# Kernel optimization log

Hardware: AMD Instinct MI355X
Metric: run time of the kernel (lower is better)

The kernel has to match this reference:

```python
import jax, jax.numpy as jnp
import numpy as np

B, S, D, H = 8, 1024, 768, 12
DH = D // H  # per-head dim = 64


def setup_inputs() -> dict:
    key = jax.random.key(0)
    ks = jax.random.split(key, 9)
    scale = 1.0 / np.sqrt(D)
    x = jax.random.normal(ks[0], (B, S, D), dtype=jnp.float32)
    # Per-head projection weights stacked over the head axis [H, D, DH]
    Wq = jax.random.normal(ks[1], (H, D, DH), dtype=jnp.float32) * scale
    bq = jax.random.normal(ks[2], (H, DH), dtype=jnp.float32) * 0.02
    Wk = jax.random.normal(ks[3], (H, D, DH), dtype=jnp.float32) * scale
    bk = jax.random.normal(ks[4], (H, DH), dtype=jnp.float32) * 0.02
    Wv = jax.random.normal(ks[5], (H, D, DH), dtype=jnp.float32) * scale
    bv = jax.random.normal(ks[6], (H, DH), dtype=jnp.float32) * 0.02
    Wo = jax.random.normal(ks[7], (D, D), dtype=jnp.float32) * scale
    bo = jax.random.normal(ks[8], (D,), dtype=jnp.float32) * 0.02
    return {"x": x, "Wq": Wq, "bq": bq, "Wk": Wk, "bk": bk,
            "Wv": Wv, "bv": bv, "Wo": Wo, "bo": bo}


def reference(x, Wq, bq, Wk, bk, Wv, bv, Wo, bo):
    # Batched equivalent of the per-head Python loop: each head has its own
    # Q/K/V linear projections (weights stacked on the head axis).
    q = jnp.einsum('bsd,hde->bhse', x, Wq) + bq[None, :, None, :]
    k = jnp.einsum('bsd,hde->bhse', x, Wk) + bk[None, :, None, :]
    v = jnp.einsum('bsd,hde->bhse', x, Wv) + bv[None, :, None, :]
    scores = jnp.einsum('bhse,bhte->bhst', q, k) / jnp.sqrt(jnp.float32(DH))
    attn = jax.nn.softmax(scores, axis=-1)
    out = jnp.einsum('bhst,bhte->bhse', attn, v)  # [B,H,S,DH]
    # concat heads on last dim -> [B,S,H*DH] = [B,S,D]
    out = out.transpose(0, 2, 1, 3).reshape(B, S, D)
    return out @ Wo.T + bo
```

## Files before the change

kernel.cpp:

```cpp
#include <hip/hip_runtime.h>
#include <hip/hip_bf16.h>


typedef unsigned short u16;
typedef unsigned int u32;
typedef __attribute__((ext_vector_type(8))) short bf16x8;
typedef __attribute__((ext_vector_type(8))) unsigned short u16x8;
typedef __attribute__((ext_vector_type(4))) float f32x4;
typedef __attribute__((ext_vector_type(4))) u32 u32x4;

typedef __attribute__((address_space(1))) const u32* gas_u32;
typedef __attribute__((address_space(3))) u32* las_u32;

#define DEVI __device__ __forceinline__

DEVI u16 f2bf(float f) {
  union { float f; u32 u; } v; v.f = f;
  u32 r = v.u + 0x7fffu + ((v.u >> 16) & 1u);
  return (u16)(r >> 16);
}

DEVI void gll16(const void* g, void* l) {
  __builtin_amdgcn_global_load_lds((gas_u32)g, (las_u32)l, 16, 0, 0);
}

DEVI f32x4 mfma16(bf16x8 a, bf16x8 b, f32x4 c) {
  return __builtin_amdgcn_mfma_f32_16x16x32_bf16(a, b, c, 0, 0, 0);
}

DEVI u32 cvtpk(float lo, float hi) {
  u32 r;
  asm("v_cvt_pk_bf16_f32 %0, %1, %2" : "=v"(r) : "v"(lo), "v"(hi));
  return r;
}

__global__ __launch_bounds__(256) void k_conv(const float* __restrict__ in,
                                              u16* __restrict__ out, int n4) {
  int i = blockIdx.x * 256 + threadIdx.x;
  if (i >= n4) return;
  float4 v = ((const float4*)in)[i];
  ushort4 o;
  o.x = f2bf(v.x); o.y = f2bf(v.y); o.z = f2bf(v.z); o.w = f2bf(v.w);
  ((ushort4*)out)[i] = o;
}

__global__ __launch_bounds__(256) void k_transW(const float* __restrict__ Wq,
                                                const float* __restrict__ Wk,
                                                const float* __restrict__ Wv,
                                                u16* __restrict__ Wtb) {
  __shared__ u16 T[64][65];
  const int th = blockIdx.y;
  const float* W = (th < 12) ? Wq : (th < 24) ? Wk : Wv;
  const int h = th % 12;
  W += (size_t)h * 768 * 64;
  const int k0 = blockIdx.x * 64;
  const int tid = threadIdx.x;
  const int row = tid >> 2, c = tid & 3;
  const float* src = W + (size_t)(k0 + row) * 64 + c * 16;
#pragma unroll
  for (int j = 0; j < 4; ++j) {
    float4 v = ((const float4*)src)[j];
    T[row][c * 16 + j * 4 + 0] = f2bf(v.x);
    T[row][c * 16 + j * 4 + 1] = f2bf(v.y);
    T[row][c * 16 + j * 4 + 2] = f2bf(v.z);
    T[row][c * 16 + j * 4 + 3] = f2bf(v.w);
  }
  __syncthreads();
  const int e = tid >> 2;
  u16* dst = Wtb + ((size_t)th * 64 + e) * 768 + k0 + c * 16;
  alignas(16) u16 tmp[16];
#pragma unroll
  for (int j = 0; j < 16; ++j) tmp[j] = T[c * 16 + j][e];
  *(u16x8*)(dst)     = *(const u16x8*)(tmp);
  *(u16x8*)(dst + 8) = *(const u16x8*)(tmp + 8);
}

template <int MODE>
__global__ __launch_bounds__(256) void k_gemm(const u16* __restrict__ Ab,
                                              const u16* __restrict__ Bb,
                                              const float* __restrict__ bias,
                                              void* __restrict__ outp) {
  __shared__ u16 smem[12288];
  u16* As = smem;
  u16* Bs = smem + 128 * 64;
  const int tid = threadIdx.x;
  const int w = tid >> 6, lane = tid & 63, lq = lane & 15, g = lane >> 4;
  const int wm = w >> 1, wn = w & 1;
  const int m0 = blockIdx.x * 128;
  const int pn = blockIdx.y;
  const u16* Brows = Bb + (size_t)pn * 64 * 768;

  f32x4 acc[4][2];
#pragma unroll
  for (int mf = 0; mf < 4; ++mf)
#pragma unroll
    for (int nf = 0; nf < 2; ++nf) acc[mf][nf] = (f32x4){0.f, 0.f, 0.f, 0.f};

  for (int kt = 0; kt < 12; ++kt) {
    const int kb = kt * 64;
#pragma unroll
    for (int i = 0; i < 4; ++i) {
      int c = w * 4 + i;
      int id = c * 64 + lane;
      int row = id >> 3, cb = id & 7;
      gll16(Ab + (size_t)(m0 + row) * 768 + kb + ((cb ^ (row & 7)) << 3), As + c * 512);
    }
#pragma unroll
    for (int i = 0; i < 2; ++i) {
      int c = w * 2 + i;
      int id = c * 64 + lane;
      int row = id >> 3, cb = id & 7;
      gll16(Brows + (size_t)row * 768 + kb + ((cb ^ (row & 7)) << 3), Bs + c * 512);
    }
    __syncthreads();
#pragma unroll
    for (int kk = 0; kk < 2; ++kk) {
      bf16x8 a[4], b[2];
#pragma unroll
      for (int mf = 0; mf < 4; ++mf) {
        int row = wm * 64 + mf * 16 + lq;
        a[mf] = *(const bf16x8*)(As + row * 64 + (((kk * 64 + g * 16) ^ ((row & 7) << 4)) >> 1));
      }
#pragma unroll
      for (int nf = 0; nf < 2; ++nf) {
        int row = wn * 32 + nf * 16 + lq;
        b[nf] = *(const bf16x8*)(Bs + row * 64 + (((kk * 64 + g * 16) ^ ((row & 7) << 4)) >> 1));
      }
#pragma unroll
      for (int mf = 0; mf < 4; ++mf)
#pragma unroll
        for (int nf = 0; nf < 2; ++nf)
          acc[mf][nf] = mfma16(a[mf], b[nf], acc[mf][nf]);
    }
    __syncthreads();
  }

  if (MODE <= 1) {
    u16* out = (u16*)outp;
    const float qs = (MODE == 0) ? 0.18033688f : 1.0f;
    const int b = m0 >> 10;
#pragma unroll
    for (int nf = 0; nf < 2; ++nf) {
      const int e = wn * 32 + nf * 16 + lq;
      const float bi = bias[pn * 64 + e];
#pragma unroll
      for (int mf = 0; mf < 4; ++mf)
#pragma unroll
        for (int r = 0; r < 4; ++r) {
          int s = (m0 & 1023) + wm * 64 + mf * 16 + 4 * g + r;
          out[((size_t)(b * 12 + pn) * 1024 + s) * 64 + e] = f2bf((acc[mf][nf][r] + bi) * qs);
        }
    }
  } else if (MODE == 2) {
    u16* Ct = smem;
#pragma unroll
    for (int nf = 0; nf < 2; ++nf) {
      const int e = wn * 32 + nf * 16 + lq;
      const float bi = bias[pn * 64 + e];
#pragma unroll
      for (int mf = 0; mf < 4; ++mf)
#pragma unroll
        for (int r = 0; r < 4; ++r) {
          int sl = wm * 64 + mf * 16 + 4 * g + r;
          Ct[e * 136 + sl] = f2bf(acc[mf][nf][r] + bi);
        }
    }
    __syncthreads();
    const int b = m0 >> 10;
    const int er = tid >> 2, cc = tid & 3;
    u16* dst = (u16*)outp + ((size_t)(b * 12 + pn) * 64 + er) * 1024 + (m0 & 1023) + cc * 32;
#pragma unroll
    for (int i = 0; i < 4; ++i)
      *(u16x8*)(dst + i * 8) = *(const u16x8*)(Ct + er * 136 + cc * 32 + i * 8);
  } else {
    float* out = (float*)outp;
#pragma unroll
    for (int nf = 0; nf < 2; ++nf) {
      const int n = pn * 64 + wn * 32 + nf * 16 + lq;
      const float bi = bias[n];
#pragma unroll
      for (int mf = 0; mf < 4; ++mf)
#pragma unroll
        for (int r = 0; r < 4; ++r) {
          int m = m0 + wm * 64 + mf * 16 + 4 * g + r;
          out[(size_t)m * 768 + n] = acc[mf][nf][r] + bi;
        }
    }
  }
}

__global__ __launch_bounds__(256) void k_attn(const u16* __restrict__ Qb,
                                              const u16* __restrict__ Kb,
                                              const u16* __restrict__ VTb,
                                              u16* __restrict__ AO) {
  __shared__ u16 Ksm[2][4096];
  __shared__ u16 Vsm[2][4096];
  const int tid = threadIdx.x;
  const int w = tid >> 6, lane = tid & 63, lq = lane & 15, g = lane >> 4;
  const int bh = blockIdx.y, b = bh / 12, h = bh % 12;
  const int q0 = blockIdx.x * 64 + w * 16;
  const u16* Qw = Qb + ((size_t)bh * 1024 + q0) * 64;
  const u16* Kp = Kb + (size_t)bh * 65536;
  const u16* Vp = VTb + (size_t)bh * 65536;
  const bool gsel = (g & 1);

  bf16x8 qf[2];
#pragma unroll
  for (int kk = 0; kk < 2; ++kk)
    qf[kk] = *(const bf16x8*)(Qw + lq * 64 + kk * 32 + g * 8);

  f32x4 o[4];
#pragma unroll
  for (int ef = 0; ef < 4; ++ef) o[ef] = (f32x4){0.f, 0.f, 0.f, 0.f};
  float l_ = 0.f;

#define STAGE(buf, kt_)                                                          \
  {                                                                              \
    const int kb_ = (kt_) * 64;                                                  \
    _Pragma("unroll")                                                            \
    for (int i = 0; i < 2; ++i) {                                                \
      int c = w * 2 + i;                                                         \
      int id = c * 64 + lane;                                                    \
      int row = id >> 3, cb = id & 7;                                            \
      int sb = cb ^ (row & 7);                                                   \
      int tb = (sb & 4) | ((sb & 1) << 1) | ((sb >> 1) & 1);                     \
      gll16(Kp + (size_t)(kb_ + row) * 64 + (sb << 3), &Ksm[buf][c * 512]);      \
      gll16(Vp + (size_t)row * 1024 + kb_ + (tb << 3), &Vsm[buf][c * 512]);      \
    }                                                                            \
  }

#define TILE(buf)                                                                \
  {                                                                              \
    f32x4 s[4];                                                                  \
    _Pragma("unroll")                                                            \
    for (int kf = 0; kf < 4; ++kf) s[kf] = (f32x4){0.f, 0.f, 0.f, 0.f};          \
    __builtin_amdgcn_s_setprio(1);                                               \
    _Pragma("unroll")                                                            \
    for (int kf = 0; kf < 4; ++kf) {                                             \
      const int row = kf * 16 + lq;                                              \
      _Pragma("unroll")                                                          \
      for (int kk = 0; kk < 2; ++kk) {                                           \
        bf16x8 kfr = *(const bf16x8*)(&Ksm[buf][0] + row * 64 +                  \
                                      (((kk * 64 + g * 16) ^ ((row & 7) << 4)) >> 1)); \
        s[kf] = mfma16(kfr, qf[kk], s[kf]);                                      \
      }                                                                          \
    }                                                                            \
    __builtin_amdgcn_s_setprio(0);                                               \
    float sm = 0.f;                                                              \
    _Pragma("unroll")                                                            \
    for (int kf = 0; kf < 4; ++kf)                                               \
      _Pragma("unroll")                                                          \
      for (int r = 0; r < 4; ++r) {                                              \
        float p = __builtin_amdgcn_exp2f(s[kf][r]);                              \
        s[kf][r] = p;                                                            \
        sm += p;                                                                 \
      }                                                                          \
    l_ += sm;                                                                    \
    u32 D[4][2];                                                                 \
    _Pragma("unroll")                                                            \
    for (int kf = 0; kf < 4; ++kf) {                                             \
      D[kf][0] = cvtpk(s[kf][0], s[kf][1]);                                      \
      D[kf][1] = cvtpk(s[kf][2], s[kf][3]);                                      \
    }                                                                            \
    _Pragma("unroll")                                                            \
    for (int kk = 0; kk < 2; ++kk) {                                             \
      const int kk2 = kk * 2;                                                    \
      u32 sa0 = gsel ? D[kk2][0] : D[kk2 + 1][0];                                \
      u32 sa1 = gsel ? D[kk2][1] : D[kk2 + 1][1];                                \
      u32 xa0 = __shfl_xor(sa0, 16), xa1 = __shfl_xor(sa1, 16);                  \
      u32x4 t = { gsel ? xa0 : D[kk2][0],                                        \
                  gsel ? xa1 : D[kk2][1],                                        \
                  gsel ? D[kk2 + 1][0] : xa0,                                    \
                  gsel ? D[kk2 + 1][1] : xa1 };                                  \
      bf16x8 pb = __builtin_bit_cast(bf16x8, t);                                 \
      __builtin_amdgcn_s_setprio(1);                                             \
      _Pragma("unroll")                                                          \
      for (int ef = 0; ef < 4; ++ef) {                                           \
        const int row = ef * 16 + lq;                                            \
        bf16x8 vf = *(const bf16x8*)(&Vsm[buf][0] + row * 64 +                   \
                                     (((kk * 64 + g * 16) ^ ((row & 7) << 4)) >> 1)); \
        o[ef] = mfma16(vf, pb, o[ef]);                                           \
      }                                                                          \
      __builtin_amdgcn_s_setprio(0);                                             \
    }                                                                            \
  }

  STAGE(0, 0)
  asm volatile("s_waitcnt vmcnt(0)" ::: "memory");
  __syncthreads();

  for (int it = 0; it < 8; ++it) {
    const int kt = it * 2;
    STAGE(1, kt + 1)
    TILE(0)
    asm volatile("s_waitcnt vmcnt(0)" ::: "memory");
    __syncthreads();
    if (it < 7) STAGE(0, kt + 2)
    TILE(1)
    asm volatile("s_waitcnt vmcnt(0)" ::: "memory");
    __syncthreads();
  }

  l_ += __shfl_xor(l_, 16);
  l_ += __shfl_xor(l_, 32);

  const float inv = 1.0f / l_;
  u16* dst = AO + ((size_t)(b * 1024 + q0 + lq)) * 768 + h * 64 + g * 4;
#pragma unroll
  for (int ef = 0; ef < 4; ++ef) {
    ushort4 t;
    t.x = f2bf(o[ef][0] * inv);
    t.y = f2bf(o[ef][1] * inv);
    t.z = f2bf(o[ef][2] * inv);
    t.w = f2bf(o[ef][3] * inv);
    *(ushort4*)(dst + ef * 16) = t;
  }
#undef STAGE
#undef TILE
}

extern "C" void kernel_launch(void* const* d_in, const int* in_sizes, int n_in,
                              void* d_out, int out_size, void* d_ws, size_t ws_size,
                              hipStream_t stream) {
  (void)in_sizes; (void)n_in; (void)out_size; (void)ws_size;
  const float* x  = (const float*)d_in[0];
  const float* Wq = (const float*)d_in[1];
  const float* bq = (const float*)d_in[2];
  const float* Wk = (const float*)d_in[3];
  const float* bk = (const float*)d_in[4];
  const float* Wv = (const float*)d_in[5];
  const float* bv = (const float*)d_in[6];
  const float* Wo = (const float*)d_in[7];
  const float* bo = (const float*)d_in[8];

  char* ws = (char*)d_ws;
  u16* xb  = (u16*)(ws);
  u16* Wtb = (u16*)(ws + 12582912);
  u16* Wob = (u16*)(ws + 12582912 + 3538944);
  u16* Qb  = (u16*)(ws + 12582912 + 3538944 + 1179648);
  u16* Kb  = Qb + (size_t)96 * 1024 * 64;
  u16* VTb = Kb + (size_t)96 * 1024 * 64;
  u16* AO  = xb;

  k_conv<<<6291456 / 1024, 256, 0, stream>>>(x, xb, 6291456 / 4);
  k_conv<<<589824 / 1024, 256, 0, stream>>>(Wo, Wob, 589824 / 4);
  k_transW<<<dim3(12, 36), 256, 0, stream>>>(Wq, Wk, Wv, Wtb);

  k_gemm<0><<<dim3(64, 12), 256, 0, stream>>>(xb, Wtb,                        bq, (void*)Qb);
  k_gemm<1><<<dim3(64, 12), 256, 0, stream>>>(xb, Wtb + (size_t)589824,       bk, (void*)Kb);
  k_gemm<2><<<dim3(64, 12), 256, 0, stream>>>(xb, Wtb + (size_t)2 * 589824,   bv, (void*)VTb);

  k_attn<<<dim3(16, 96), 256, 0, stream>>>(Qb, Kb, VTb, AO);

  k_gemm<3><<<dim3(64, 12), 256, 0, stream>>>(AO, Wob, bo, d_out);
}
```

Before: 123.1 us.

## Merge Q/K projections into one GEMM, compute V^T directly, widen tiles and attention blocks

The GEMM tile grows from 128x64 to 128x128. Q and K are computed in one launch that writes to two outputs, and V^T comes from a swapped-operand GEMM (W_v times x) instead of staging a transpose through LDS. The output projection uses the wider tile on a 64x6 grid. The attention kernel moves to 512 threads per block with 128 queries each, so every K/V tile in LDS is shared by twice as many queries. This cuts launches and redundant operand loads, but leaves fewer blocks per GEMM, uses more registers for accumulators, and writes V^T with scattered scalar stores.

```diff
diff --git a/kernel.cpp b/kernel.cpp
--- a/kernel.cpp
+++ b/kernel.cpp
@@ -76,25 +76,27 @@
 }
 
 template <int MODE>
-__global__ __launch_bounds__(256) void k_gemm(const u16* __restrict__ Ab,
-                                              const u16* __restrict__ Bb,
-                                              const float* __restrict__ bias,
-                                              void* __restrict__ outp) {
-  __shared__ u16 smem[12288];
+__global__ __launch_bounds__(256) void k_gemm2(const u16* __restrict__ Ab,
+                                               const u16* __restrict__ Bb,
+                                               const float* __restrict__ b0,
+                                               const float* __restrict__ b1,
+                                               void* __restrict__ outp) {
+  __shared__ u16 smem[16384];
   u16* As = smem;
-  u16* Bs = smem + 128 * 64;
+  u16* Bs = smem + 8192;
   const int tid = threadIdx.x;
   const int w = tid >> 6, lane = tid & 63, lq = lane & 15, g = lane >> 4;
   const int wm = w >> 1, wn = w & 1;
-  const int m0 = blockIdx.x * 128;
-  const int pn = blockIdx.y;
-  const u16* Brows = Bb + (size_t)pn * 64 * 768;
-
-  f32x4 acc[4][2];
+  const int pm = blockIdx.x, pn = blockIdx.y;
+  const int m0 = pm * 128;
+  const u16* Arows = Ab + (size_t)m0 * 768;
+  const u16* Brows = Bb + (size_t)pn * 128 * 768;
+
+  f32x4 acc[4][4];
 #pragma unroll
   for (int mf = 0; mf < 4; ++mf)
 #pragma unroll
-    for (int nf = 0; nf < 2; ++nf) acc[mf][nf] = (f32x4){0.f, 0.f, 0.f, 0.f};
+    for (int nf = 0; nf < 4; ++nf) acc[mf][nf] = (f32x4){0.f, 0.f, 0.f, 0.f};
 
   for (int kt = 0; kt < 12; ++kt) {
     const int kb = kt * 64;
@@ -103,81 +105,75 @@
       int c = w * 4 + i;
       int id = c * 64 + lane;
       int row = id >> 3, cb = id & 7;
-      gll16(Ab + (size_t)(m0 + row) * 768 + kb + ((cb ^ (row & 7)) << 3), As + c * 512);
-    }
-#pragma unroll
-    for (int i = 0; i < 2; ++i) {
-      int c = w * 2 + i;
-      int id = c * 64 + lane;
-      int row = id >> 3, cb = id & 7;
-      gll16(Brows + (size_t)row * 768 + kb + ((cb ^ (row & 7)) << 3), Bs + c * 512);
+      int sw = (cb ^ (row & 7)) << 3;
+      gll16(Arows + (size_t)row * 768 + kb + sw, As + c * 512);
+      gll16(Brows + (size_t)row * 768 + kb + sw, Bs + c * 512);
     }
     __syncthreads();
 #pragma unroll
     for (int kk = 0; kk < 2; ++kk) {
-      bf16x8 a[4], b[2];
+      bf16x8 a[4], b[4];
 #pragma unroll
       for (int mf = 0; mf < 4; ++mf) {
         int row = wm * 64 + mf * 16 + lq;
         a[mf] = *(const bf16x8*)(As + row * 64 + (((kk * 64 + g * 16) ^ ((row & 7) << 4)) >> 1));
       }
 #pragma unroll
-      for (int nf = 0; nf < 2; ++nf) {
-        int row = wn * 32 + nf * 16 + lq;
+      for (int nf = 0; nf < 4; ++nf) {
+        int row = wn * 64 + nf * 16 + lq;
         b[nf] = *(const bf16x8*)(Bs + row * 64 + (((kk * 64 + g * 16) ^ ((row & 7) << 4)) >> 1));
       }
 #pragma unroll
       for (int mf = 0; mf < 4; ++mf)
 #pragma unroll
-        for (int nf = 0; nf < 2; ++nf)
+        for (int nf = 0; nf < 4; ++nf)
           acc[mf][nf] = mfma16(a[mf], b[nf], acc[mf][nf]);
     }
     __syncthreads();
   }
 
-  if (MODE <= 1) {
-    u16* out = (u16*)outp;
-    const float qs = (MODE == 0) ? 0.18033688f : 1.0f;
+  if (MODE == 0) {
+    const int t = (pn >= 6) ? 1 : 0;
+    const float qs = t ? 1.0f : 0.18033688f;
+    const float* bp = t ? b1 : b0;
+    const int pn6 = pn - t * 6;
+    u16* out = (u16*)outp + (size_t)t * 6291456;
     const int b = m0 >> 10;
 #pragma unroll
-    for (int nf = 0; nf < 2; ++nf) {
-      const int e = wn * 32 + nf * 16 + lq;
-      const float bi = bias[pn * 64 + e];
+    for (int nf = 0; nf < 4; ++nf) {
+      const int n = pn6 * 128 + wn * 64 + nf * 16 + lq;
+      const int h = n >> 6, e = n & 63;
+      const float bi = bp[n];
 #pragma unroll
       for (int mf = 0; mf < 4; ++mf)
 #pragma unroll
         for (int r = 0; r < 4; ++r) {
           int s = (m0 & 1023) + wm * 64 + mf * 16 + 4 * g + r;
-          out[((size_t)(b * 12 + pn) * 1024 + s) * 64 + e] = f2bf((acc[mf][nf][r] + bi) * qs);
+          out[((size_t)(b * 12 + h) << 16) + s * 64 + e] = f2bf((acc[mf][nf][r] + bi) * qs);
         }
     }
-  } else if (MODE == 2) {
-    u16* Ct = smem;
-#pragma unroll
-    for (int nf = 0; nf < 2; ++nf) {
-      const int e = wn * 32 + nf * 16 + lq;
-      const float bi = bias[pn * 64 + e];
-#pragma unroll
-      for (int mf = 0; mf < 4; ++mf)
-#pragma unroll
-        for (int r = 0; r < 4; ++r) {
-          int sl = wm * 64 + mf * 16 + 4 * g + r;
-          Ct[e * 136 + sl] = f2bf(acc[mf][nf][r] + bi);
+  } else if (MODE == 1) {
+    u16* out = (u16*)outp;
+#pragma unroll
+    for (int mf = 0; mf < 4; ++mf)
+#pragma unroll
+      for (int r = 0; r < 4; ++r) {
+        const int m = m0 + wm * 64 + mf * 16 + 4 * g + r;
+        const float bi = b0[m];
+        const int h = m >> 6, e = m & 63;
+#pragma unroll
+        for (int nf = 0; nf < 4; ++nf) {
+          const int n = pn * 128 + wn * 64 + nf * 16 + lq;
+          const int b = n >> 10, s = n & 1023;
+          out[((size_t)(b * 12 + h) << 16) + e * 1024 + s] = f2bf(acc[mf][nf][r] + bi);
         }
-    }
-    __syncthreads();
-    const int b = m0 >> 10;
-    const int er = tid >> 2, cc = tid & 3;
-    u16* dst = (u16*)outp + ((size_t)(b * 12 + pn) * 64 + er) * 1024 + (m0 & 1023) + cc * 32;
-#pragma unroll
-    for (int i = 0; i < 4; ++i)
-      *(u16x8*)(dst + i * 8) = *(const u16x8*)(Ct + er * 136 + cc * 32 + i * 8);
+      }
   } else {
     float* out = (float*)outp;
 #pragma unroll
-    for (int nf = 0; nf < 2; ++nf) {
-      const int n = pn * 64 + wn * 32 + nf * 16 + lq;
-      const float bi = bias[n];
+    for (int nf = 0; nf < 4; ++nf) {
+      const int n = pn * 128 + wn * 64 + nf * 16 + lq;
+      const float bi = b0[n];
 #pragma unroll
       for (int mf = 0; mf < 4; ++mf)
 #pragma unroll
@@ -189,7 +185,7 @@
   }
 }
 
-__global__ __launch_bounds__(256) void k_attn(const u16* __restrict__ Qb,
+__global__ __launch_bounds__(512) void k_attn(const u16* __restrict__ Qb,
                                               const u16* __restrict__ Kb,
                                               const u16* __restrict__ VTb,
                                               u16* __restrict__ AO) {
@@ -198,7 +194,7 @@
   const int tid = threadIdx.x;
   const int w = tid >> 6, lane = tid & 63, lq = lane & 15, g = lane >> 4;
   const int bh = blockIdx.y, b = bh / 12, h = bh % 12;
-  const int q0 = blockIdx.x * 64 + w * 16;
+  const int q0 = blockIdx.x * 128 + w * 16;
   const u16* Qw = Qb + ((size_t)bh * 1024 + q0) * 64;
   const u16* Kp = Kb + (size_t)bh * 65536;
   const u16* Vp = VTb + (size_t)bh * 65536;
@@ -217,16 +213,12 @@
 #define STAGE(buf, kt_)                                                          \
   {                                                                              \
     const int kb_ = (kt_) * 64;                                                  \
-    _Pragma("unroll")                                                            \
-    for (int i = 0; i < 2; ++i) {                                                \
-      int c = w * 2 + i;                                                         \
-      int id = c * 64 + lane;                                                    \
-      int row = id >> 3, cb = id & 7;                                            \
-      int sb = cb ^ (row & 7);                                                   \
-      int tb = (sb & 4) | ((sb & 1) << 1) | ((sb >> 1) & 1);                     \
-      gll16(Kp + (size_t)(kb_ + row) * 64 + (sb << 3), &Ksm[buf][c * 512]);      \
-      gll16(Vp + (size_t)row * 1024 + kb_ + (tb << 3), &Vsm[buf][c * 512]);      \
-    }                                                                            \
+    const int id = w * 64 + lane;                                                \
+    const int row = id >> 3, cb = id & 7;                                        \
+    const int sb = cb ^ (row & 7);                                               \
+    const int tb = (sb & 4) | ((sb & 1) << 1) | ((sb >> 1) & 1);                 \
+    gll16(Kp + (size_t)(kb_ + row) * 64 + (sb << 3), &Ksm[buf][w * 512]);        \
+    gll16(Vp + (size_t)row * 1024 + kb_ + (tb << 3), &Vsm[buf][w * 512]);        \
   }
 
 #define TILE(buf)                                                                \
@@ -346,11 +338,10 @@
   k_conv<<<589824 / 1024, 256, 0, stream>>>(Wo, Wob, 589824 / 4);
   k_transW<<<dim3(12, 36), 256, 0, stream>>>(Wq, Wk, Wv, Wtb);
 
-  k_gemm<0><<<dim3(64, 12), 256, 0, stream>>>(xb, Wtb,                        bq, (void*)Qb);
-  k_gemm<1><<<dim3(64, 12), 256, 0, stream>>>(xb, Wtb + (size_t)589824,       bk, (void*)Kb);
-  k_gemm<2><<<dim3(64, 12), 256, 0, stream>>>(xb, Wtb + (size_t)2 * 589824,   bv, (void*)VTb);
-
-  k_attn<<<dim3(16, 96), 256, 0, stream>>>(Qb, Kb, VTb, AO);
-
-  k_gemm<3><<<dim3(64, 12), 256, 0, stream>>>(AO, Wob, bo, d_out);
-}
+  k_gemm2<0><<<dim3(64, 12), 256, 0, stream>>>(xb, Wtb, bq, bk, (void*)Qb);
+  k_gemm2<1><<<dim3(6, 64), 256, 0, stream>>>(Wtb + (size_t)1536 * 768, xb, bv, nullptr, (void*)VTb);
+
+  k_attn<<<dim3(8, 96), 512, 0, stream>>>(Qb, Kb, VTb, AO);
+
+  k_gemm2<2><<<dim3(64, 6), 256, 0, stream>>>(AO, Wob, bo, nullptr, d_out);
+}
```

After: 130.2 us. 5.7% more time.
